# Kernel optimization log

Measured on AMD Instinct MI355X. Metric: run time of the kernel, lower is better.

The kernel has to match this reference:

```python
import jax, jax.numpy as jnp
import numpy as np

N_NODES = 50000


def gcn_conv(x, W, b, src, dst, n_nodes):
    # PyG GCNConv: h = W x; out = D^{-1/2} (A + I) D^{-1/2} h + b
    h = x @ W  # [N, out_dim]
    ones = jnp.ones(src.shape[0], dtype=x.dtype)
    # degree with self-loops, counted on destination nodes
    deg = jax.ops.segment_sum(ones, dst, num_segments=n_nodes) + 1.0
    dinv = jax.lax.rsqrt(deg)  # deg >= 1, always safe
    norm = dinv[src] * dinv[dst]  # [E]
    agg = jax.ops.segment_sum(h[src] * norm[:, None], dst, num_segments=n_nodes)
    agg = agg + h * (dinv * dinv)[:, None]  # self-loop contribution
    return agg + b


def setup_inputs() -> dict:
    key = jax.random.key(0)
    k1, k2, k3, k4 = jax.random.split(key, 4)
    input_dim, hidden_dim, output_dim = 512, 256, 64
    n_edges = 1_600_000
    x = jax.random.normal(k1, (N_NODES, input_dim), dtype=jnp.float32)
    edge_index = jax.random.randint(k2, (2, n_edges), 0, N_NODES, dtype=jnp.int32)
    W1 = jax.random.normal(k3, (input_dim, hidden_dim), dtype=jnp.float32) / np.sqrt(input_dim)
    b1 = jnp.zeros((hidden_dim,), dtype=jnp.float32)
    W2 = jax.random.normal(k4, (hidden_dim, output_dim), dtype=jnp.float32) / np.sqrt(hidden_dim)
    b2 = jnp.zeros((output_dim,), dtype=jnp.float32)
    return {"x": x, "W1": W1, "b1": b1, "W2": W2, "b2": b2, "edge_index": edge_index}


def reference(x, W1, b1, W2, b2, edge_index):
    src, dst = edge_index[0], edge_index[1]
    h = jax.nn.relu(gcn_conv(x, W1, b1, src, dst, N_NODES))
    h = gcn_conv(h, W2, b2, src, dst, N_NODES)
    return jax.nn.log_softmax(h, axis=1)
```

## Files before the change

### kernel.cpp

```cpp
#include <hip/hip_runtime.h>

#define NODES 50000
#define NBIN 196
#define EPB 4096

typedef __attribute__((ext_vector_type(8))) short short8;
typedef __attribute__((ext_vector_type(4))) float f32x4;
typedef __attribute__((ext_vector_type(2))) float f32x2;

__device__ __forceinline__ ushort f2bf(float f) {
    uint u = __float_as_uint(f);
    uint r = (u + 0x7fffu + ((u >> 16) & 1u)) >> 16;
    return (ushort)r;
}
__device__ __forceinline__ float bf2f(ushort u) {
    return __uint_as_float(((uint)u) << 16);
}
__device__ __forceinline__ uchar f2fp8(float f) {
    return (uchar)(__builtin_amdgcn_cvt_pk_fp8_f32(f, f, 0, false) & 0xff);
}
__device__ __forceinline__ uint cvtpk_bf16(float lo, float hi) {
    uint r;
    asm("v_cvt_pk_bf16_f32 %0, %1, %2" : "=v"(r) : "v"(lo), "v"(hi));
    return r;
}


__global__ __launch_bounds__(256) void k_hist(const int* __restrict__ dst, int E,
                                              int* __restrict__ hist, int nblk) {
    __shared__ int h[NBIN];
    int t = threadIdx.x;
    for (int i = t; i < NBIN; i += 256) h[i] = 0;
    __syncthreads();
    int base = blockIdx.x * EPB;
#pragma unroll
    for (int i = 0; i < EPB / 256; ++i) {
        int e = base + i * 256 + t;
        if (e < E) atomicAdd(&h[dst[e] >> 8], 1);
    }
    __syncthreads();
    for (int i = t; i < NBIN; i += 256) hist[i * nblk + blockIdx.x] = h[i];
}

__global__ __launch_bounds__(1024) void k_scanbin(const int* __restrict__ hist,
                                                  int* __restrict__ offl,
                                                  int* __restrict__ btot, int nblk) {
    __shared__ int s[1024];
    int b = blockIdx.x, t = threadIdx.x;
    int v = (t < nblk) ? hist[b * nblk + t] : 0;
    s[t] = v;
    __syncthreads();
    for (int off = 1; off < 1024; off <<= 1) {
        int u = (t >= off) ? s[t - off] : 0;
        __syncthreads();
        s[t] += u;
        __syncthreads();
    }
    if (t < nblk) offl[b * nblk + t] = s[t] - v;
    if (t == 1023) btot[b] = s[1023];
}

__global__ __launch_bounds__(256) void k_scanoff(const int* __restrict__ btot,
                                                 int* __restrict__ binoff,
                                                 int* __restrict__ rowstart, int E) {
    __shared__ int s[256];
    int t = threadIdx.x;
    int v = (t < NBIN) ? btot[t] : 0;
    s[t] = v;
    __syncthreads();
    for (int off = 1; off < 256; off <<= 1) {
        int u = (t >= off) ? s[t - off] : 0;
        __syncthreads();
        s[t] += u;
        __syncthreads();
    }
    if (t < NBIN) binoff[t] = s[t] - v;
    if (t == 0) { binoff[NBIN] = E; rowstart[NODES] = E; }
}

__global__ __launch_bounds__(256) void k_part(const int* __restrict__ src,
                                              const int* __restrict__ dst, int E,
                                              const int* __restrict__ offl,
                                              const int* __restrict__ binoff, int nblk,
                                              uint* __restrict__ tmp) {
    __shared__ int cur[NBIN];
    int t = threadIdx.x, blk = blockIdx.x;
    for (int i = t; i < NBIN; i += 256) cur[i] = binoff[i] + offl[i * nblk + blk];
    __syncthreads();
    int base = blk * EPB;
#pragma unroll
    for (int i = 0; i < EPB / 256; ++i) {
        int e = base + i * 256 + t;
        if (e < E) {
            int d = dst[e];
            int p = atomicAdd(&cur[d >> 8], 1);
            tmp[p] = (uint)src[e] | ((uint)(d & 0xff) << 16);
        }
    }
}

__global__ __launch_bounds__(256) void k_csr(const uint* __restrict__ tmp,
                                             const int* __restrict__ binoff,
                                             int* __restrict__ rowstart,
                                             float* __restrict__ dinv,
                                             ushort* __restrict__ esrc16) {
    __shared__ int ncnt[256], nst[256];
    int b = blockIdx.x, t = threadIdx.x;
    int e0 = binoff[b], e1 = binoff[b + 1];
    int nb0 = b << 8;
    int nn = min(256, NODES - nb0);
    ncnt[t] = 0;
    __syncthreads();
    for (int e = e0 + t; e < e1; e += 256) atomicAdd(&ncnt[(tmp[e] >> 16) & 0xff], 1);
    __syncthreads();
    int v = ncnt[t];
    nst[t] = v;
    __syncthreads();
    for (int off = 1; off < 256; off <<= 1) {
        int u = (t >= off) ? nst[t - off] : 0;
        __syncthreads();
        nst[t] += u;
        __syncthreads();
    }
    int excl = nst[t] - v;
    if (t < nn) {
        rowstart[nb0 + t] = e0 + excl;
        dinv[nb0 + t] = rsqrtf(1.0f + (float)v);
    }
    __syncthreads();
    ncnt[t] = e0 + excl;
    __syncthreads();
    for (int e = e0 + t; e < e1; e += 256) {
        uint q = tmp[e];
        int p = atomicAdd(&ncnt[(q >> 16) & 0xff], 1);
        esrc16[p] = (ushort)(q & 0xffff);
    }
}

__global__ void k_wfill(const ushort* __restrict__ esrc16, const float* __restrict__ dinv,
                        uint* __restrict__ epack, int E) {
    int e4 = (blockIdx.x * blockDim.x + threadIdx.x) * 4;
    if (e4 + 3 < E) {
        ushort4 s = *(const ushort4*)(esrc16 + e4);
        uint4 o;
        o.x = (uint)s.x | ((uint)f2bf(dinv[s.x]) << 16);
        o.y = (uint)s.y | ((uint)f2bf(dinv[s.y]) << 16);
        o.z = (uint)s.z | ((uint)f2bf(dinv[s.z]) << 16);
        o.w = (uint)s.w | ((uint)f2bf(dinv[s.w]) << 16);
        *(uint4*)(epack + e4) = o;
    } else {
        for (int e = e4; e < E; ++e) {
            int s = esrc16[e];
            epack[e] = (uint)s | ((uint)f2bf(dinv[s]) << 16);
        }
    }
}

__global__ void k_cast2(const float* __restrict__ W1, ushort* __restrict__ w1t,
                        const float* __restrict__ W2, ushort* __restrict__ w2t) {
    const int N1 = 512 * 256;
    int i = blockIdx.x * blockDim.x + threadIdx.x;
    if (i < N1) {
        int r = i / 256, c = i % 256;
        w1t[(size_t)c * 512 + r] = f2bf(W1[i]);
    } else {
        int j = i - N1;
        if (j < 256 * 64) {
            int r = j / 64, c = j % 64;
            w2t[(size_t)c * 256 + r] = f2bf(W2[j]);
        }
    }
}

__global__ __launch_bounds__(256) void k_gemm1(const float* __restrict__ x,
                                               const ushort* __restrict__ w1t,
                                               uchar* __restrict__ h1f8, int M, int K) {
    constexpr int BM = 64, BN = 128, BK = 64;
    constexpr int NIT = 8;
    __shared__ __align__(16) ushort As[BM * BK];
    __shared__ __align__(16) ushort Bs[BN * BK];

    int t = threadIdx.x;
    int w = t >> 6, l = t & 63;
    int wm = w & 1, wn = w >> 1;
    int bm = (blockIdx.x >> 1) * BM;
    int bn = (blockIdx.x & 1) * BN;
    int lr = l & 15, g4 = l >> 4;

    f32x4 acc[2][4] = {};

    int ar = t >> 2;
    int aq = t & 3;
    int arow_g = bm + ar;
    bool aok = arow_g < M;
    const float* ap = x + (size_t)arow_g * K + aq * 16;
    char* adst = (char*)As + ar * 128;
    int aswz = (ar & 7) << 4;

    int brow_loc = l >> 3;
    int bseg = ((l & 7) << 4) ^ (brow_loc << 4);

    float4 fa[4];
    auto loadA = [&](int k0) {
#pragma unroll
        for (int j = 0; j < 4; ++j)
            fa[j] = aok ? *(const float4*)(ap + k0 + j * 4) : make_float4(0.f, 0.f, 0.f, 0.f);
    };
    auto writeA = [&]() {
#pragma unroll
        for (int j = 0; j < 2; ++j) {
            uint p0 = cvtpk_bf16(fa[2 * j].x, fa[2 * j].y);
            uint p1 = cvtpk_bf16(fa[2 * j].z, fa[2 * j].w);
            uint p2 = cvtpk_bf16(fa[2 * j + 1].x, fa[2 * j + 1].y);
            uint p3 = cvtpk_bf16(fa[2 * j + 1].z, fa[2 * j + 1].w);
            int4 v = make_int4((int)p0, (int)p1, (int)p2, (int)p3);
            *(int4*)(adst + ((aq * 32 + j * 16) ^ aswz)) = v;
        }
    };
    auto stageB = [&](int k0) {
#pragma unroll
        for (int i = 0; i < 4; ++i) {
            int rbase = w * 32 + i * 8;
            const char* gsrc = (const char*)w1t + (size_t)(bn + rbase + brow_loc) * (K * 2) + k0 * 2 + bseg;
            __builtin_amdgcn_global_load_lds(
                (const __attribute__((address_space(1))) uint*)gsrc,
                (__attribute__((address_space(3))) uint*)((char*)Bs + rbase * 128),
                16, 0, 0);
        }
    };
    auto compute = [&]() {
#pragma unroll
        for (int ks = 0; ks < 2; ++ks) {
            short8 af[2], bfr[4];
#pragma unroll
            for (int mt = 0; mt < 2; ++mt) {
                int r = wm * 32 + mt * 16 + lr;
                af[mt] = *(const short8*)((const char*)As + r * 128 + ((ks * 64 + g4 * 16) ^ ((r & 7) << 4)));
            }
#pragma unroll
            for (int nt = 0; nt < 4; ++nt) {
                int r = wn * 64 + nt * 16 + lr;
                bfr[nt] = *(const short8*)((const char*)Bs + r * 128 + ((ks * 64 + g4 * 16) ^ ((r & 7) << 4)));
            }
#pragma unroll
            for (int mt = 0; mt < 2; ++mt)
#pragma unroll
                for (int nt = 0; nt < 4; ++nt)
                    acc[mt][nt] = __builtin_amdgcn_mfma_f32_16x16x32_bf16(af[mt], bfr[nt], acc[mt][nt], 0, 0, 0);
        }
    };

    loadA(0);
    stageB(0);
    writeA();
    __syncthreads();

    for (int it = 0; it < NIT; ++it) {
        if (it + 1 < NIT) loadA((it + 1) * BK);
        compute();
        if (it + 1 < NIT) {
            __syncthreads();
            stageB((it + 1) * BK);
            writeA();
            __syncthreads();
        }
    }

#pragma unroll
    for (int mt = 0; mt < 2; ++mt)
#pragma unroll
        for (int nt = 0; nt < 4; ++nt)
#pragma unroll
            for (int i = 0; i < 4; ++i) {
                int row = bm + wm * 32 + mt * 16 + g4 * 4 + i;
                int col = bn + wn * 64 + nt * 16 + lr;
                if (row < M) h1f8[(size_t)row * 256 + col] = f2fp8(acc[mt][nt][i]);
            }
}

__global__ __launch_bounds__(256) void k_agg1g2(const uchar* __restrict__ h8,
                                                const int* __restrict__ rowstart,
                                                const uint* __restrict__ ep,
                                                const float* __restrict__ dinv,
                                                const float* __restrict__ b1,
                                                const ushort* __restrict__ w2t,
                                                ushort* __restrict__ h2b) {
    __shared__ __align__(16) ushort rows[16 * 256];
    int t = threadIdx.x;
    int w = __builtin_amdgcn_readfirstlane(t >> 6);
    int lane = t & 63;
    int nb = blockIdx.x * 16;
    const uchar* hl = h8 + lane * 4;

    for (int i = 0; i < 4; ++i) {
        int r = w * 4 + i;
        int n = nb + r;
        float4 acc = make_float4(0.f, 0.f, 0.f, 0.f);
        int e0 = __builtin_amdgcn_readfirstlane(rowstart[n]);
        int e1 = __builtin_amdgcn_readfirstlane(rowstart[n + 1]);
        int e = e0;
#define A1_STEP(q, qv)                                                        \
        {                                                                     \
            float wt = __uint_as_float((q) & 0xffff0000u);                    \
            f32x2 lo = __builtin_amdgcn_cvt_pk_f32_fp8((int)(qv), false);     \
            f32x2 hi = __builtin_amdgcn_cvt_pk_f32_fp8((int)(qv), true);      \
            acc.x = fmaf(wt, lo[0], acc.x);                                   \
            acc.y = fmaf(wt, lo[1], acc.y);                                   \
            acc.z = fmaf(wt, hi[0], acc.z);                                   \
            acc.w = fmaf(wt, hi[1], acc.w);                                   \
        }
        for (; e + 8 <= e1; e += 8) {
            uint q0 = ep[e],     q1 = ep[e + 1], q2 = ep[e + 2], q3 = ep[e + 3];
            uint q4 = ep[e + 4], q5 = ep[e + 5], q6 = ep[e + 6], q7 = ep[e + 7];
            uint v0 = *(const uint*)(hl + (size_t)(q0 & 0xffff) * 256);
            uint v1 = *(const uint*)(hl + (size_t)(q1 & 0xffff) * 256);
            uint v2 = *(const uint*)(hl + (size_t)(q2 & 0xffff) * 256);
            uint v3 = *(const uint*)(hl + (size_t)(q3 & 0xffff) * 256);
            uint v4 = *(const uint*)(hl + (size_t)(q4 & 0xffff) * 256);
            uint v5 = *(const uint*)(hl + (size_t)(q5 & 0xffff) * 256);
            uint v6 = *(const uint*)(hl + (size_t)(q6 & 0xffff) * 256);
            uint v7 = *(const uint*)(hl + (size_t)(q7 & 0xffff) * 256);
            A1_STEP(q0, v0) A1_STEP(q1, v1) A1_STEP(q2, v2) A1_STEP(q3, v3)
            A1_STEP(q4, v4) A1_STEP(q5, v5) A1_STEP(q6, v6) A1_STEP(q7, v7)
        }
        for (; e < e1; ++e) {
            uint q = ep[e];
            uint v = *(const uint*)(hl + (size_t)(q & 0xffff) * 256);
            A1_STEP(q, v)
        }
#undef A1_STEP
        float dn = dinv[n];
        float s2v = dn * dn;
        uint qs = *(const uint*)(hl + (size_t)n * 256);
        f32x2 slo = __builtin_amdgcn_cvt_pk_f32_fp8((int)qs, false);
        f32x2 shi = __builtin_amdgcn_cvt_pk_f32_fp8((int)qs, true);
        float4 bb = *(const float4*)(b1 + lane * 4);
        float rx = fmaxf(fmaf(acc.x, dn, fmaf(slo[0], s2v, bb.x)), 0.f);
        float ry = fmaxf(fmaf(acc.y, dn, fmaf(slo[1], s2v, bb.y)), 0.f);
        float rz = fmaxf(fmaf(acc.z, dn, fmaf(shi[0], s2v, bb.z)), 0.f);
        float rw = fmaxf(fmaf(acc.w, dn, fmaf(shi[1], s2v, bb.w)), 0.f);
        uint p0 = cvtpk_bf16(rx, ry);
        uint p1 = cvtpk_bf16(rz, rw);
        *(uint2*)((char*)rows + r * 512 + ((lane * 8) ^ ((r & 7) << 4))) =
            make_uint2(p0, p1);
    }
    __syncthreads();

    int lr = lane & 15, g4 = lane >> 4;
    f32x4 acc2 = {};
    const ushort* bcol = w2t + (size_t)(w * 16 + lr) * 256;
#pragma unroll
    for (int ks = 0; ks < 8; ++ks) {
        short8 af = *(const short8*)((const char*)rows + lr * 512 +
                                     ((ks * 64 + g4 * 16) ^ ((lr & 7) << 4)));
        short8 bf = *(const short8*)(bcol + ks * 32 + g4 * 8);
        acc2 = __builtin_amdgcn_mfma_f32_16x16x32_bf16(af, bf, acc2, 0, 0, 0);
    }
#pragma unroll
    for (int i = 0; i < 4; ++i) {
        int node = nb + g4 * 4 + i;
        h2b[(size_t)node * 64 + w * 16 + lr] = f2bf(acc2[i]);
    }
}

__global__ __launch_bounds__(256) void k_agg2(const ushort* __restrict__ h,
                                              const int* __restrict__ rowstart,
                                              const uint* __restrict__ ep,
                                              const float* __restrict__ dinv,
                                              const float* __restrict__ b2,
                                              float* __restrict__ out) {
    int wave = __builtin_amdgcn_readfirstlane(threadIdx.x >> 6);
    int lane = threadIdx.x & 63;
    int n = blockIdx.x * 4 + wave;
    if (n >= NODES) return;
    const ushort* hl = h + lane;
    float acc = 0.f;
    int e0 = __builtin_amdgcn_readfirstlane(rowstart[n]);
    int e1 = __builtin_amdgcn_readfirstlane(rowstart[n + 1]);
    int e = e0;
    for (; e + 8 <= e1; e += 8) {
        uint q0 = ep[e],     q1 = ep[e + 1], q2 = ep[e + 2], q3 = ep[e + 3];
        uint q4 = ep[e + 4], q5 = ep[e + 5], q6 = ep[e + 6], q7 = ep[e + 7];
        float v0 = bf2f(hl[(size_t)(q0 & 0xffff) * 64]);
        float v1 = bf2f(hl[(size_t)(q1 & 0xffff) * 64]);
        float v2 = bf2f(hl[(size_t)(q2 & 0xffff) * 64]);
        float v3 = bf2f(hl[(size_t)(q3 & 0xffff) * 64]);
        float v4 = bf2f(hl[(size_t)(q4 & 0xffff) * 64]);
        float v5 = bf2f(hl[(size_t)(q5 & 0xffff) * 64]);
        float v6 = bf2f(hl[(size_t)(q6 & 0xffff) * 64]);
        float v7 = bf2f(hl[(size_t)(q7 & 0xffff) * 64]);
        acc = fmaf(__uint_as_float(q0 & 0xffff0000u), v0, acc);
        acc = fmaf(__uint_as_float(q1 & 0xffff0000u), v1, acc);
        acc = fmaf(__uint_as_float(q2 & 0xffff0000u), v2, acc);
        acc = fmaf(__uint_as_float(q3 & 0xffff0000u), v3, acc);
        acc = fmaf(__uint_as_float(q4 & 0xffff0000u), v4, acc);
        acc = fmaf(__uint_as_float(q5 & 0xffff0000u), v5, acc);
        acc = fmaf(__uint_as_float(q6 & 0xffff0000u), v6, acc);
        acc = fmaf(__uint_as_float(q7 & 0xffff0000u), v7, acc);
    }
    for (; e < e1; ++e) {
        uint q = ep[e];
        acc = fmaf(__uint_as_float(q & 0xffff0000u), bf2f(hl[(size_t)(q & 0xffff) * 64]), acc);
    }
    float dn = dinv[n];
    float r = fmaf(acc, dn, fmaf(bf2f(hl[(size_t)n * 64]), dn * dn, b2[lane]));
    float m = r;
#pragma unroll
    for (int off = 32; off; off >>= 1) m = fmaxf(m, __shfl_xor(m, off));
    float ex = __expf(r - m);
    float ssum = ex;
#pragma unroll
    for (int off = 32; off; off >>= 1) ssum += __shfl_xor(ssum, off);
    out[(size_t)n * 64 + lane] = r - m - __logf(ssum);
}


extern "C" void kernel_launch(void* const* d_in, const int* in_sizes, int n_in,
                              void* d_out, int out_size, void* d_ws, size_t ws_size,
                              hipStream_t stream) {
    const float* x  = (const float*)d_in[0];
    const float* W1 = (const float*)d_in[1];
    const float* b1 = (const float*)d_in[2];
    const float* W2 = (const float*)d_in[3];
    const float* b2 = (const float*)d_in[4];
    const int*   ei = (const int*)d_in[5];
    int E = in_sizes[5] / 2;
    const int* src = ei;
    const int* dst = ei + E;
    float* out = (float*)d_out;

    int nblk = (E + EPB - 1) / EPB;

    char* wsp = (char*)d_ws;
    auto alloc = [&](size_t bytes) {
        char* p = wsp;
        wsp += (bytes + 255) & ~(size_t)255;
        return p;
    };
    int*    hist     = (int*)alloc((size_t)NBIN * nblk * 4);
    int*    offl     = (int*)alloc((size_t)NBIN * nblk * 4);
    int*    btot     = (int*)alloc((size_t)NBIN * 4);
    int*    binoff   = (int*)alloc((size_t)(NBIN + 1) * 4);
    int*    rowstart = (int*)alloc((size_t)(NODES + 1) * 4);
    float*  dinv     = (float*)alloc((size_t)NODES * 4);
    uint*   tmp      = (uint*)alloc((size_t)E * 4);
    ushort* esrc16   = (ushort*)alloc((size_t)E * 2);
    uint*   epack    = (uint*)alloc((size_t)E * 4);
    ushort* w1t      = (ushort*)alloc((size_t)256 * 512 * 2);
    ushort* w2t      = (ushort*)alloc((size_t)64 * 256 * 2);
    uchar*  h1f8     = (uchar*)alloc((size_t)NODES * 256);
    ushort* h2b      = (ushort*)alloc((size_t)NODES * 64 * 2);

    k_hist<<<nblk, 256, 0, stream>>>(dst, E, hist, nblk);
    k_scanbin<<<NBIN, 1024, 0, stream>>>(hist, offl, btot, nblk);
    k_scanoff<<<1, 256, 0, stream>>>(btot, binoff, rowstart, E);
    k_part<<<nblk, 256, 0, stream>>>(src, dst, E, offl, binoff, nblk, tmp);
    k_csr<<<NBIN, 256, 0, stream>>>(tmp, binoff, rowstart, dinv, esrc16);
    k_wfill<<<(E / 4 + 255) / 256, 256, 0, stream>>>(esrc16, dinv, epack, E);

    k_cast2<<<(512 * 256 + 256 * 64 + 255) / 256, 256, 0, stream>>>(W1, w1t, W2, w2t);

    k_gemm1<<<((NODES + 63) / 64) * 2, 256, 0, stream>>>(x, w1t, h1f8, NODES, 512);

    k_agg1g2<<<NODES / 16, 256, 0, stream>>>(h1f8, rowstart, epack, dinv, b1, w2t, h2b);

    k_agg2<<<(NODES + 3) / 4, 256, 0, stream>>>(h2b, rowstart, epack, dinv, b2, out);
}
```

Before: 197.0 us.

## Split layer-1 gather across lane groups processing four edges per instruction

The aggregation kernel now splits each wavefront into four 16-lane groups. Each group gathers a different edge's 64-byte feature slice, and the row is covered in four quarter passes, with partial sums reduced via shuffles. The goal is more edges in flight per load instruction and more memory-level parallelism. In exchange, the edge list and rowstart are read four times, shuffle reductions are added, and each gather touches smaller fragments.

```diff
diff --git a/kernel.cpp b/kernel.cpp
--- a/kernel.cpp
+++ b/kernel.cpp
@@ -289,60 +289,69 @@
     int t = threadIdx.x;
     int w = __builtin_amdgcn_readfirstlane(t >> 6);
     int lane = t & 63;
+    int g = lane >> 4;
+    int d4 = lane & 15;
     int nb = blockIdx.x * 16;
-    const uchar* hl = h8 + lane * 4;
-
-    for (int i = 0; i < 4; ++i) {
-        int r = w * 4 + i;
-        int n = nb + r;
-        float4 acc = make_float4(0.f, 0.f, 0.f, 0.f);
-        int e0 = __builtin_amdgcn_readfirstlane(rowstart[n]);
-        int e1 = __builtin_amdgcn_readfirstlane(rowstart[n + 1]);
-        int e = e0;
-#define A1_STEP(q, qv)                                                        \
-        {                                                                     \
-            float wt = __uint_as_float((q) & 0xffff0000u);                    \
-            f32x2 lo = __builtin_amdgcn_cvt_pk_f32_fp8((int)(qv), false);     \
-            f32x2 hi = __builtin_amdgcn_cvt_pk_f32_fp8((int)(qv), true);      \
-            acc.x = fmaf(wt, lo[0], acc.x);                                   \
-            acc.y = fmaf(wt, lo[1], acc.y);                                   \
-            acc.z = fmaf(wt, hi[0], acc.z);                                   \
-            acc.w = fmaf(wt, hi[1], acc.w);                                   \
-        }
-        for (; e + 8 <= e1; e += 8) {
-            uint q0 = ep[e],     q1 = ep[e + 1], q2 = ep[e + 2], q3 = ep[e + 3];
-            uint q4 = ep[e + 4], q5 = ep[e + 5], q6 = ep[e + 6], q7 = ep[e + 7];
-            uint v0 = *(const uint*)(hl + (size_t)(q0 & 0xffff) * 256);
-            uint v1 = *(const uint*)(hl + (size_t)(q1 & 0xffff) * 256);
-            uint v2 = *(const uint*)(hl + (size_t)(q2 & 0xffff) * 256);
-            uint v3 = *(const uint*)(hl + (size_t)(q3 & 0xffff) * 256);
-            uint v4 = *(const uint*)(hl + (size_t)(q4 & 0xffff) * 256);
-            uint v5 = *(const uint*)(hl + (size_t)(q5 & 0xffff) * 256);
-            uint v6 = *(const uint*)(hl + (size_t)(q6 & 0xffff) * 256);
-            uint v7 = *(const uint*)(hl + (size_t)(q7 & 0xffff) * 256);
-            A1_STEP(q0, v0) A1_STEP(q1, v1) A1_STEP(q2, v2) A1_STEP(q3, v3)
-            A1_STEP(q4, v4) A1_STEP(q5, v5) A1_STEP(q6, v6) A1_STEP(q7, v7)
-        }
-        for (; e < e1; ++e) {
-            uint q = ep[e];
-            uint v = *(const uint*)(hl + (size_t)(q & 0xffff) * 256);
-            A1_STEP(q, v)
-        }
+
+    for (int q = 0; q < 4; ++q) {
+        const uchar* hq = h8 + q * 64 + d4 * 4;
+        for (int i = 0; i < 4; ++i) {
+            int r = w * 4 + i;
+            int n = nb + r;
+            float4 acc = make_float4(0.f, 0.f, 0.f, 0.f);
+            int e0 = __builtin_amdgcn_readfirstlane(rowstart[n]);
+            int e1 = __builtin_amdgcn_readfirstlane(rowstart[n + 1]);
+            int e = e0;
+#define A1_STEP(qr, qv)                                                       \
+            {                                                                 \
+                float wt = __uint_as_float((qr) & 0xffff0000u);               \
+                f32x2 lo = __builtin_amdgcn_cvt_pk_f32_fp8((int)(qv), false); \
+                f32x2 hi = __builtin_amdgcn_cvt_pk_f32_fp8((int)(qv), true);  \
+                acc.x = fmaf(wt, lo[0], acc.x);                               \
+                acc.y = fmaf(wt, lo[1], acc.y);                               \
+                acc.z = fmaf(wt, hi[0], acc.z);                               \
+                acc.w = fmaf(wt, hi[1], acc.w);                               \
+            }
+            for (; e + 8 <= e1; e += 8) {
+                uint qa = ep[e + g];
+                uint qb = ep[e + 4 + g];
+                uint va = *(const uint*)(hq + (size_t)(qa & 0xffff) * 256);
+                uint vb = *(const uint*)(hq + (size_t)(qb & 0xffff) * 256);
+                A1_STEP(qa, va)
+                A1_STEP(qb, vb)
+            }
+            for (; e < e1; e += 4) {
+                int ee = e + g;
+                if (ee < e1) {
+                    uint qr = ep[ee];
+                    uint v = *(const uint*)(hq + (size_t)(qr & 0xffff) * 256);
+                    A1_STEP(qr, v)
+                }
+            }
 #undef A1_STEP
-        float dn = dinv[n];
-        float s2v = dn * dn;
-        uint qs = *(const uint*)(hl + (size_t)n * 256);
-        f32x2 slo = __builtin_amdgcn_cvt_pk_f32_fp8((int)qs, false);
-        f32x2 shi = __builtin_amdgcn_cvt_pk_f32_fp8((int)qs, true);
-        float4 bb = *(const float4*)(b1 + lane * 4);
-        float rx = fmaxf(fmaf(acc.x, dn, fmaf(slo[0], s2v, bb.x)), 0.f);
-        float ry = fmaxf(fmaf(acc.y, dn, fmaf(slo[1], s2v, bb.y)), 0.f);
-        float rz = fmaxf(fmaf(acc.z, dn, fmaf(shi[0], s2v, bb.z)), 0.f);
-        float rw = fmaxf(fmaf(acc.w, dn, fmaf(shi[1], s2v, bb.w)), 0.f);
-        uint p0 = cvtpk_bf16(rx, ry);
-        uint p1 = cvtpk_bf16(rz, rw);
-        *(uint2*)((char*)rows + r * 512 + ((lane * 8) ^ ((r & 7) << 4))) =
-            make_uint2(p0, p1);
+            acc.x += __shfl_xor(acc.x, 16); acc.y += __shfl_xor(acc.y, 16);
+            acc.z += __shfl_xor(acc.z, 16); acc.w += __shfl_xor(acc.w, 16);
+            acc.x += __shfl_xor(acc.x, 32); acc.y += __shfl_xor(acc.y, 32);
+            acc.z += __shfl_xor(acc.z, 32); acc.w += __shfl_xor(acc.w, 32);
+
+            if (lane < 16) {
+                float dn = dinv[n];
+                float s2v = dn * dn;
+                uint qs = *(const uint*)(hq + (size_t)n * 256);
+                f32x2 slo = __builtin_amdgcn_cvt_pk_f32_fp8((int)qs, false);
+                f32x2 shi = __builtin_amdgcn_cvt_pk_f32_fp8((int)qs, true);
+                const float* bq = b1 + q * 64 + d4 * 4;
+                float4 bb = *(const float4*)bq;
+                float rx = fmaxf(fmaf(acc.x, dn, fmaf(slo[0], s2v, bb.x)), 0.f);
+                float ry = fmaxf(fmaf(acc.y, dn, fmaf(slo[1], s2v, bb.y)), 0.f);
+                float rz = fmaxf(fmaf(acc.z, dn, fmaf(shi[0], s2v, bb.z)), 0.f);
+                float rw = fmaxf(fmaf(acc.w, dn, fmaf(shi[1], s2v, bb.w)), 0.f);
+                uint p0 = cvtpk_bf16(rx, ry);
+                uint p1 = cvtpk_bf16(rz, rw);
+                *(uint2*)((char*)rows + r * 512 + ((q * 128 + d4 * 8) ^ ((r & 7) << 4))) =
+                    make_uint2(p0, p1);
+            }
+        }
     }
     __syncthreads();
 
```

Result: slower. 278.0 us (+41.1%).
